# Optimization experiments

Measured on AMD Instinct MI355X. Metric: run time of the kernel, lower is better.

The kernel has to match this reference:

```python
import jax, jax.numpy as jnp
import numpy as np

B, S, D, H, L, K = 16, 512, 256, 8, 4, 16
N, E, NE = B * S, 65536, 32768
DFF = 2 * D
HD = D // H


def _layer_norm(x, g, b):
    mu = jnp.mean(x, axis=-1, keepdims=True)
    var = jnp.mean(jnp.square(x - mu), axis=-1, keepdims=True)
    return (x - mu) / jnp.sqrt(var + 1e-5) * g + b


def setup_inputs() -> dict:
    key = jax.random.key(0)
    ks = iter(jax.random.split(key, 32))
    p = lambda shape: jax.random.normal(next(ks), shape, dtype=jnp.float32) * 0.02
    inp = {
        "node_embedding": jax.random.normal(next(ks), (N, D), dtype=jnp.float32),
        "edge_embedding": jax.random.normal(next(ks), (E, D), dtype=jnp.float32),
        "incidence": jax.random.randint(next(ks), (2, E), 0, N),
        "src_key_padding_mask": jnp.zeros((B, S), dtype=bool),
        "edges_neg": jax.random.randint(next(ks), (NE, 2), 0, N),
        "edges_pos": jax.random.randint(next(ks), (NE, 2), 0, N),
        # ConcatenateLinear(D, D, D): y = x1 @ W1^T + x2 @ W2^T + b
        "msg_w1": p((D, D)), "msg_w2": p((D, D)), "msg_b": p((D,)),
        "pos_table": p((S, D)),
        # per-layer transformer params, stacked on leading L axis
        "in_proj_w": p((L, 3 * D, D)), "in_proj_b": p((L, 3 * D)),
        "out_w": p((L, D, D)), "out_b": p((L, D)),
        "ln1_g": jnp.ones((L, D), jnp.float32), "ln1_b": jnp.zeros((L, D), jnp.float32),
        "ff_w1": p((L, DFF, D)), "ff_b1": p((L, DFF)),
        "ff_w2": p((L, D, DFF)), "ff_b2": p((L, D)),
        "ln2_g": jnp.ones((L, D), jnp.float32), "ln2_b": jnp.zeros((L, D), jnp.float32),
        "pe_w": p((1, D)), "pe_b": p((1,)),
        "pt_w": p((K, D)), "pt_b": p((K,)),
    }
    return inp


def reference(node_embedding, edge_embedding, incidence, src_key_padding_mask,
              edges_neg, edges_pos, msg_w1, msg_w2, msg_b, pos_table,
              in_proj_w, in_proj_b, out_w, out_b, ln1_g, ln1_b,
              ff_w1, ff_b1, ff_w2, ff_b2, ln2_g, ln2_b,
              pe_w, pe_b, pt_w, pt_b):
    # --- aggregate_by_incidence: gather -> ConcatenateLinear -> scatter-add ---
    msgs = (node_embedding[incidence[1]] @ msg_w1.T
            + edge_embedding @ msg_w2.T + msg_b)            # [E, D]
    agreg = jnp.zeros_like(node_embedding).at[incidence[0]].add(msgs)

    # positional encoding tiled over the batch (positions = arange(lMax))
    x = node_embedding + agreg + jnp.tile(pos_table, (B, 1))
    x = x.reshape(B, S, D)

    mask_bias = jnp.where(src_key_padding_mask, -1e9, 0.0)[:, None, None, :]  # [B,1,1,S]
    scale = 1.0 / jnp.sqrt(jnp.float32(HD))

    # post-norm TransformerEncoder (dropout=0 at eval), relu FFN
    for i in range(L):
        wq, wk, wv = jnp.split(in_proj_w[i], 3, axis=0)
        bq, bk, bv = jnp.split(in_proj_b[i], 3, axis=0)
        q = (x @ wq.T + bq).reshape(B, S, H, HD)
        k = (x @ wk.T + bk).reshape(B, S, H, HD)
        v = (x @ wv.T + bv).reshape(B, S, H, HD)
        scores = jnp.einsum('bqhd,bkhd->bhqk', q, k) * scale + mask_bias
        a = jax.nn.softmax(scores, axis=-1)
        o = jnp.einsum('bhqk,bkhd->bqhd', a, v).reshape(B, S, D)
        o = o @ out_w[i].T + out_b[i]
        x = _layer_norm(x + o, ln1_g[i], ln1_b[i])
        h = jax.nn.relu(x @ ff_w1[i].T + ff_b1[i]) @ ff_w2[i].T + ff_b2[i]
        x = _layer_norm(x + h, ln2_g[i], ln2_b[i])

    # --- representation_final_edges: gather pairs, elementwise product ---
    flat = x.reshape(B * S, D)
    rep_pos = flat[edges_pos[:, 0]] * flat[edges_pos[:, 1]]
    rep_neg = flat[edges_neg[:, 0]] * flat[edges_neg[:, 1]]

    pred_pos = rep_pos @ pe_w.T + pe_b      # [NE, 1]
    pred_neg = rep_neg @ pe_w.T + pe_b      # [NE, 1]
    pred_type = rep_pos @ pt_w.T + pt_b     # [NE, K]
    return (pred_pos, pred_neg, pred_type)
```

## Files before the change

kernel.cpp:

```cpp
#include <hip/hip_runtime.h>
#include <hip/hip_bf16.h>

#define B_  16
#define S_  512
#define D_  256
#define H_  8
#define L_  4
#define K_  16
#define N_  (B_ * S_)
#define E_  65536
#define NE_ 32768
#define DFF_ 512
#define HD_ 32

typedef __attribute__((ext_vector_type(8))) __bf16 bf16x8;
typedef __attribute__((ext_vector_type(4))) __bf16 bf16x4;
typedef __attribute__((ext_vector_type(4))) float f32x4;

__device__ __forceinline__ void gl2lds16(const void* g, void* l) {
    __builtin_amdgcn_global_load_lds(
        (const __attribute__((address_space(1))) unsigned int*)g,
        (__attribute__((address_space(3))) unsigned int*)l, 16, 0, 0);
}

#define QSCALE 0.17677669529663688f

__global__ __launch_bounds__(256) void convert_all(
    const float* __restrict__ ipw, __bf16* __restrict__ ipw_bf,
    const float* __restrict__ ow,  __bf16* __restrict__ ow_bf,
    const float* __restrict__ fw1, __bf16* __restrict__ fw1_bf,
    const float* __restrict__ fw2, __bf16* __restrict__ fw2_bf,
    const float* __restrict__ mw1, const float* __restrict__ mw2,
    __bf16* __restrict__ wcat_bf,
    const float* __restrict__ ptw, const float* __restrict__ pew,
    __bf16* __restrict__ wp_bf,
    const float* __restrict__ ipb, float* __restrict__ ipb_s,
    int* __restrict__ cnt)
{
    int blk = blockIdx.x;
    if (blk < 768) {
        size_t i = ((size_t)blk * 256 + threadIdx.x) * 4;
        int row = (int)((i >> 8) % 768);
        float sc = (row < 256) ? QSCALE : 1.0f;
        float4 v = *(const float4*)(ipw + i);
        bf16x4 o = {(__bf16)(v.x * sc), (__bf16)(v.y * sc),
                    (__bf16)(v.z * sc), (__bf16)(v.w * sc)};
        *(bf16x4*)(ipw_bf + i) = o;
    } else if (blk < 2048) {
        const float* src; __bf16* dst; int base;
        if      (blk < 1024)  { src = ow;   dst = ow_bf;   base = blk - 768; }
        else if (blk < 1536)  { src = fw1;  dst = fw1_bf;  base = blk - 1024; }
        else                  { src = fw2;  dst = fw2_bf;  base = blk - 1536; }
        size_t i = ((size_t)base * 256 + threadIdx.x) * 4;
        float4 v = *(const float4*)(src + i);
        bf16x4 o = {(__bf16)v.x, (__bf16)v.y, (__bf16)v.z, (__bf16)v.w};
        *(bf16x4*)(dst + i) = o;
    } else if (blk < 2176) {
        int isw2 = blk >= 2112;
        int base = blk - (isw2 ? 2112 : 2048);
        const float* src = isw2 ? mw2 : mw1;
        size_t i = ((size_t)base * 256 + threadIdx.x) * 4;
        int row = i >> 8, col = i & 255;
        float4 v = *(const float4*)(src + i);
        bf16x4 o = {(__bf16)v.x, (__bf16)v.y, (__bf16)v.z, (__bf16)v.w};
        *(bf16x4*)(wcat_bf + (size_t)row * 512 + (isw2 ? 256 : 0) + col) = o;
    } else if (blk < 2184) {
        int base = blk - 2176;
        size_t i = ((size_t)base * 256 + threadIdx.x) * 4;
        int row = i >> 8, col = i & 255;
        float4 v = make_float4(0.f, 0.f, 0.f, 0.f);
        if (row < 16)       v = *(const float4*)(ptw + row * 256 + col);
        else if (row == 16) v = *(const float4*)(pew + col);
        bf16x4 o = {(__bf16)v.x, (__bf16)v.y, (__bf16)v.z, (__bf16)v.w};
        *(bf16x4*)(wp_bf + i) = o;
    } else if (blk < 2187) {
        int base = blk - 2184;
        size_t i = ((size_t)base * 256 + threadIdx.x) * 4;
        if (i < 3072) {
            float sc = ((i % 768) < 256) ? QSCALE : 1.0f;
            float4 v = *(const float4*)(ipb + i);
            *(float4*)(ipb_s + i) = make_float4(v.x * sc, v.y * sc, v.z * sc, v.w * sc);
        }
    } else {
        int base = blk - 2187;
        int4* p = (int4*)(cnt + ((size_t)base * 256 + threadIdx.x) * 4);
        *p = make_int4(0, 0, 0, 0);
    }
}

__global__ __launch_bounds__(256) void hist_kernel(
    const int* __restrict__ inc, int* __restrict__ cnt)
{
    int e = blockIdx.x * 256 + threadIdx.x;
    atomicAdd(&cnt[inc[e]], 1);
}

__global__ __launch_bounds__(256) void scan_kernel(
    const int* __restrict__ cnt, int* __restrict__ row_ptr, int* __restrict__ ofs)
{
    __shared__ int part[256];
    int t = threadIdx.x;
    int base = t * 32, sum = 0;
    int local[32];
    #pragma unroll
    for (int j = 0; j < 32; ++j) { local[j] = cnt[base + j]; sum += local[j]; }
    part[t] = sum;
    __syncthreads();
    #pragma unroll
    for (int off = 1; off < 256; off <<= 1) {
        int other = (t >= off) ? part[t - off] : 0;
        __syncthreads();
        part[t] += other;
        __syncthreads();
    }
    int run = part[t] - sum;
    for (int j = 0; j < 32; ++j) {
        row_ptr[base + j] = run;
        ofs[base + j] = run;
        run += local[j];
    }
    if (t == 255) row_ptr[8192] = run;
}

__global__ __launch_bounds__(256) void fill_kernel(
    const int* __restrict__ inc, int* __restrict__ ofs, int* __restrict__ elist)
{
    int e = blockIdx.x * 256 + threadIdx.x;
    int pos = atomicAdd(&ofs[inc[e]], 1);
    elist[pos] = e;
}

__global__ __launch_bounds__(256) void csr_gather(
    const float* __restrict__ node, const float* __restrict__ edge,
    const int* __restrict__ inc, const int* __restrict__ row_ptr,
    const int* __restrict__ elist, __bf16* __restrict__ G)
{
    int n = blockIdx.x * 4 + (threadIdx.x >> 6);
    int lane = threadIdx.x & 63;
    int s = row_ptr[n], epos = row_ptr[n + 1];
    float4 an = {0.f, 0.f, 0.f, 0.f}, ae = {0.f, 0.f, 0.f, 0.f};
    int i = s;
    for (; i + 2 <= epos; i += 2) {
        int e0 = elist[i], e1 = elist[i + 1];
        int s0 = inc[E_ + e0], s1 = inc[E_ + e1];
        float4 nv0 = *(const float4*)(node + (size_t)s0 * 256 + lane * 4);
        float4 ev0 = *(const float4*)(edge + (size_t)e0 * 256 + lane * 4);
        float4 nv1 = *(const float4*)(node + (size_t)s1 * 256 + lane * 4);
        float4 ev1 = *(const float4*)(edge + (size_t)e1 * 256 + lane * 4);
        an.x += nv0.x + nv1.x; an.y += nv0.y + nv1.y;
        an.z += nv0.z + nv1.z; an.w += nv0.w + nv1.w;
        ae.x += ev0.x + ev1.x; ae.y += ev0.y + ev1.y;
        ae.z += ev0.z + ev1.z; ae.w += ev0.w + ev1.w;
    }
    if (i < epos) {
        int e0 = elist[i];
        int s0 = inc[E_ + e0];
        float4 nv0 = *(const float4*)(node + (size_t)s0 * 256 + lane * 4);
        float4 ev0 = *(const float4*)(edge + (size_t)e0 * 256 + lane * 4);
        an.x += nv0.x; an.y += nv0.y; an.z += nv0.z; an.w += nv0.w;
        ae.x += ev0.x; ae.y += ev0.y; ae.z += ev0.z; ae.w += ev0.w;
    }
    __bf16* g = G + (size_t)n * 512 + lane * 4;
    bf16x4 bn = {(__bf16)an.x, (__bf16)an.y, (__bf16)an.z, (__bf16)an.w};
    bf16x4 be = {(__bf16)ae.x, (__bf16)ae.y, (__bf16)ae.z, (__bf16)ae.w};
    *(bf16x4*)g = bn;
    *(bf16x4*)(g + 256) = be;
}

template <typename OutT>
__global__ __launch_bounds__(256) void gemm_mfma(
    const __bf16* __restrict__ A, const __bf16* __restrict__ Bw,
    const float* __restrict__ bias, OutT* __restrict__ C,
    int M, int N, int Kd, int relu)
{
    __shared__ __bf16 As0[64 * 32], As1[64 * 32];
    __shared__ __bf16 Bs0[128 * 32], Bs1[128 * 32];
    int tid = threadIdx.x;
    int m0 = blockIdx.y * 64, n0 = blockIdx.x * 128;
    int w = tid >> 6, lane = tid & 63, quad = lane >> 4, r16 = lane & 15;
    int wr = w >> 1, wc = w & 1;

    int lr = tid >> 2, lc = (tid & 3) * 8;
    const __bf16* ag  = A  + (size_t)(m0 + lr) * Kd + lc;
    const __bf16* bg0 = Bw + (size_t)(n0 + lr) * Kd + lc;
    const __bf16* bg1 = bg0 + (size_t)64 * Kd;

    f32x4 acc[2][4] = {};

    for (int k0 = 0; k0 < Kd; k0 += 64) {
        __syncthreads();
        gl2lds16(ag + k0,        As0 + tid * 8);
        gl2lds16(ag + k0 + 32,   As1 + tid * 8);
        gl2lds16(bg0 + k0,       Bs0 + tid * 8);
        gl2lds16(bg1 + k0,       Bs0 + 2048 + tid * 8);
        gl2lds16(bg0 + k0 + 32,  Bs1 + tid * 8);
        gl2lds16(bg1 + k0 + 32,  Bs1 + 2048 + tid * 8);
        __syncthreads();

        #pragma unroll
        for (int kh = 0; kh < 2; ++kh) {
            const __bf16* Asr = kh ? As1 : As0;
            const __bf16* Bsr = kh ? Bs1 : Bs0;
            bf16x8 af[2], bfr[4];
            #pragma unroll
            for (int mt = 0; mt < 2; ++mt)
                af[mt] = *(const bf16x8*)(Asr + (wr * 32 + mt * 16 + r16) * 32 + quad * 8);
            #pragma unroll
            for (int nt = 0; nt < 4; ++nt)
                bfr[nt] = *(const bf16x8*)(Bsr + (wc * 64 + nt * 16 + r16) * 32 + quad * 8);
            #pragma unroll
            for (int mt = 0; mt < 2; ++mt)
                #pragma unroll
                for (int nt = 0; nt < 4; ++nt)
                    acc[mt][nt] = __builtin_amdgcn_mfma_f32_16x16x32_bf16(
                        af[mt], bfr[nt], acc[mt][nt], 0, 0, 0);
        }
    }

    #pragma unroll
    for (int nt = 0; nt < 4; ++nt) {
        int n = n0 + wc * 64 + nt * 16 + r16;
        float bv = bias[n];
        #pragma unroll
        for (int mt = 0; mt < 2; ++mt) {
            #pragma unroll
            for (int reg = 0; reg < 4; ++reg) {
                int m = m0 + wr * 32 + mt * 16 + quad * 4 + reg;
                float v = acc[mt][nt][reg] + bv;
                if (relu) v = fmaxf(v, 0.f);
                C[(size_t)m * N + n] = (OutT)v;
            }
        }
    }
}

__global__ __launch_bounds__(256) void agreg_gemm(
    const __bf16* __restrict__ G, const __bf16* __restrict__ Wc,
    const int* __restrict__ row_ptr, const float* __restrict__ mb,
    const float* __restrict__ node, const float* __restrict__ pos,
    float* __restrict__ xo, __bf16* __restrict__ xo_bf)
{
    __shared__ __bf16 As0[32 * 32], As1[32 * 32];
    __shared__ __bf16 Bs0[128 * 32], Bs1[128 * 32];
    int tid = threadIdx.x;
    int m0 = blockIdx.y * 32, n0 = blockIdx.x * 128;
    int w = tid >> 6, lane = tid & 63, quad = lane >> 4, r16 = lane & 15;
    int wr = w >> 1, wc = w & 1;

    int lr = tid >> 2, lc = (tid & 3) * 8;
    const __bf16* ag  = G  + (size_t)(m0 + (tid >> 2 & 31)) * 512 + lc;
    const __bf16* bg0 = Wc + (size_t)(n0 + lr) * 512 + lc;
    const __bf16* bg1 = bg0 + (size_t)64 * 512;

    f32x4 acc[4] = {};

    for (int k0 = 0; k0 < 512; k0 += 64) {
        __syncthreads();
        if (tid < 128) {
            gl2lds16(ag + k0,      As0 + tid * 8);
            gl2lds16(ag + k0 + 32, As1 + tid * 8);
        }
        gl2lds16(bg0 + k0,       Bs0 + tid * 8);
        gl2lds16(bg1 + k0,       Bs0 + 2048 + tid * 8);
        gl2lds16(bg0 + k0 + 32,  Bs1 + tid * 8);
        gl2lds16(bg1 + k0 + 32,  Bs1 + 2048 + tid * 8);
        __syncthreads();

        #pragma unroll
        for (int kh = 0; kh < 2; ++kh) {
            const __bf16* Asr = kh ? As1 : As0;
            const __bf16* Bsr = kh ? Bs1 : Bs0;
            bf16x8 af = *(const bf16x8*)(Asr + (wr * 16 + r16) * 32 + quad * 8);
            #pragma unroll
            for (int nt = 0; nt < 4; ++nt) {
                bf16x8 bfr = *(const bf16x8*)(Bsr + (wc * 64 + nt * 16 + r16) * 32 + quad * 8);
                acc[nt] = __builtin_amdgcn_mfma_f32_16x16x32_bf16(af, bfr, acc[nt], 0, 0, 0);
            }
        }
    }

    #pragma unroll
    for (int nt = 0; nt < 4; ++nt) {
        int n = n0 + wc * 64 + nt * 16 + r16;
        float mbv = mb[n];
        #pragma unroll
        for (int reg = 0; reg < 4; ++reg) {
            int m = m0 + wr * 16 + quad * 4 + reg;
            float deg = (float)(row_ptr[m + 1] - row_ptr[m]);
            float v = acc[nt][reg] + deg * mbv
                    + node[(size_t)m * 256 + n] + pos[(size_t)(m & 511) * 256 + n];
            xo[(size_t)m * 256 + n] = v;
            xo_bf[(size_t)m * 256 + n] = (__bf16)v;
        }
    }
}

__global__ __launch_bounds__(256) void gemm_ln(
    const __bf16* __restrict__ A, const __bf16* __restrict__ W,
    const float* __restrict__ bias, const float* res,
    const float* __restrict__ g, const float* __restrict__ b,
    float* xo, __bf16* __restrict__ xo_bf, int Kd)
{
    __shared__ __bf16 As0[16 * 32], As1[16 * 32];
    __shared__ __bf16 Bs0[256 * 32], Bs1[256 * 32];
    __shared__ float redS[4][16], redQ[4][16];
    int tid = threadIdx.x;
    int m0 = blockIdx.x * 16;
    int w = tid >> 6, lane = tid & 63, quad = lane >> 4, r16 = lane & 15;

    f32x4 acc[4] = {};

    for (int k0 = 0; k0 < Kd; k0 += 64) {
        __syncthreads();
        if (tid < 64) {
            const __bf16* ap = A + (size_t)(m0 + (tid >> 2)) * Kd + (tid & 3) * 8;
            gl2lds16(ap + k0,      As0 + tid * 8);
            gl2lds16(ap + k0 + 32, As1 + tid * 8);
        }
        #pragma unroll
        for (int c = 0; c < 4; ++c) {
            const __bf16* wp = W + (size_t)(c * 64 + (tid >> 2)) * Kd + (tid & 3) * 8;
            gl2lds16(wp + k0,      Bs0 + c * 2048 + tid * 8);
            gl2lds16(wp + k0 + 32, Bs1 + c * 2048 + tid * 8);
        }
        __syncthreads();

        #pragma unroll
        for (int kh = 0; kh < 2; ++kh) {
            const __bf16* Asr = kh ? As1 : As0;
            const __bf16* Bsr = kh ? Bs1 : Bs0;
            bf16x8 af = *(const bf16x8*)(Asr + r16 * 32 + quad * 8);
            #pragma unroll
            for (int nt = 0; nt < 4; ++nt) {
                bf16x8 bfr = *(const bf16x8*)(Bsr + (w * 64 + nt * 16 + r16) * 32 + quad * 8);
                acc[nt] = __builtin_amdgcn_mfma_f32_16x16x32_bf16(af, bfr, acc[nt], 0, 0, 0);
            }
        }
    }

    float vv[4][4];
    float ls[4], lq[4];
    #pragma unroll
    for (int reg = 0; reg < 4; ++reg) {
        int m = m0 + quad * 4 + reg;
        float s = 0.f, q = 0.f;
        #pragma unroll
        for (int nt = 0; nt < 4; ++nt) {
            int col = w * 64 + nt * 16 + r16;
            float val = acc[nt][reg] + bias[col] + res[(size_t)m * 256 + col];
            vv[reg][nt] = val;
            s += val; q += val * val;
        }
        #pragma unroll
        for (int off = 1; off < 16; off <<= 1) {
            s += __shfl_xor(s, off);
            q += __shfl_xor(q, off);
        }
        ls[reg] = s; lq[reg] = q;
    }
    if (r16 == 0) {
        #pragma unroll
        for (int reg = 0; reg < 4; ++reg) {
            int r = quad * 4 + reg;
            redS[w][r] = ls[reg];
            redQ[w][r] = lq[reg];
        }
    }
    __syncthreads();

    #pragma unroll
    for (int reg = 0; reg < 4; ++reg) {
        int r = quad * 4 + reg;
        int m = m0 + r;
        float s = redS[0][r] + redS[1][r] + redS[2][r] + redS[3][r];
        float q = redQ[0][r] + redQ[1][r] + redQ[2][r] + redQ[3][r];
        float mu = s * (1.f / 256.f);
        float var = q * (1.f / 256.f) - mu * mu;
        float rstd = rsqrtf(var + 1e-5f);
        #pragma unroll
        for (int nt = 0; nt < 4; ++nt) {
            int col = w * 64 + nt * 16 + r16;
            float val = (vv[reg][nt] - mu) * rstd * g[col] + b[col];
            xo[(size_t)m * 256 + col] = val;
            xo_bf[(size_t)m * 256 + col] = (__bf16)val;
        }
    }
}

#define VS 72
#define PS 72

__global__ __launch_bounds__(256) void attn_mfma_kernel(
    const __bf16* __restrict__ qkv, __bf16* __restrict__ o)
{
    __shared__ __bf16 Vt[2][32 * VS];
    __shared__ __bf16 Ps[4][16 * PS];

    int tid  = threadIdx.x;
    int w    = tid >> 6, lane = tid & 63;
    int quad = lane >> 4, r16 = lane & 15;
    int qt = blockIdx.x;
    int bh = blockIdx.y;
    int b = bh >> 3, h = bh & 7;
    int base = b * S_;
    int q0 = qt * 64;

    bf16x8 qa = *(const bf16x8*)(
        qkv + (size_t)(base + q0 + w * 16 + r16) * 768 + h * 32 + quad * 8);

    int kp  = tid & 31;
    int cch = (tid >> 5) & 3;
    int jh  = tid >> 7;
    const __bf16* vbase = qkv + (size_t)base * 768 + 512 + h * 32 + cch * 8;
    const __bf16* kbase = qkv + (size_t)base * 768 + 256 + h * 32 + quad * 8;

    bf16x8 va  = *(const bf16x8*)(vbase + (size_t)(2 * kp) * 768);
    bf16x8 vb2 = *(const bf16x8*)(vbase + (size_t)(2 * kp + 1) * 768);
    bf16x8 kb[4], kbn[4];
    #pragma unroll
    for (int t = 0; t < 4; ++t)
        kbn[t] = *(const bf16x8*)(kbase + (size_t)(t * 16 + r16) * 768);

    f32x4 oacc0 = {0.f, 0.f, 0.f, 0.f};
    f32x4 oacc1 = {0.f, 0.f, 0.f, 0.f};
    float l_i[4] = {0.f, 0.f, 0.f, 0.f};

    for (int kt = 0; kt < 8; ++kt) {
        int buf = kt & 1;
        #pragma unroll
        for (int j = 0; j < 4; ++j) {
            int jj = jh * 4 + j;
            int d = cch * 8 + jj;
            union { __bf16 hh[2]; unsigned int u; } pk;
            pk.hh[0] = va[jj];
            pk.hh[1] = vb2[jj];
            *(unsigned int*)(&Vt[buf][d * VS + 2 * kp]) = pk.u;
        }
        #pragma unroll
        for (int t = 0; t < 4; ++t) kb[t] = kbn[t];
        __syncthreads();

        if (kt < 7) {
            int off = (kt + 1) * 64;
            va  = *(const bf16x8*)(vbase + (size_t)(off + 2 * kp) * 768);
            vb2 = *(const bf16x8*)(vbase + (size_t)(off + 2 * kp + 1) * 768);
            #pragma unroll
            for (int t = 0; t < 4; ++t)
                kbn[t] = *(const bf16x8*)(kbase + (size_t)(off + t * 16 + r16) * 768);
        }

        f32x4 s[4];
        #pragma unroll
        for (int t = 0; t < 4; ++t)
            s[t] = __builtin_amdgcn_mfma_f32_16x16x32_bf16(
                qa, kb[t], (f32x4){0.f, 0.f, 0.f, 0.f}, 0, 0, 0);

        #pragma unroll
        for (int r = 0; r < 4; ++r) {
            float p0 = __expf(s[0][r]), p1 = __expf(s[1][r]);
            float p2 = __expf(s[2][r]), p3 = __expf(s[3][r]);
            l_i[r] += (p0 + p1) + (p2 + p3);
            __bf16* pw = &Ps[w][(quad * 4 + r) * PS + r16];
            pw[0]  = (__bf16)p0;
            pw[16] = (__bf16)p1;
            pw[32] = (__bf16)p2;
            pw[48] = (__bf16)p3;
        }

        #pragma unroll
        for (int c = 0; c < 2; ++c) {
            bf16x8 pa  = *(const bf16x8*)(&Ps[w][r16 * PS + c * 32 + quad * 8]);
            bf16x8 vb0 = *(const bf16x8*)(&Vt[buf][r16 * VS + c * 32 + quad * 8]);
            bf16x8 vb1 = *(const bf16x8*)(&Vt[buf][(16 + r16) * VS + c * 32 + quad * 8]);
            oacc0 = __builtin_amdgcn_mfma_f32_16x16x32_bf16(pa, vb0, oacc0, 0, 0, 0);
            oacc1 = __builtin_amdgcn_mfma_f32_16x16x32_bf16(pa, vb1, oacc1, 0, 0, 0);
        }
    }

    #pragma unroll
    for (int r = 0; r < 4; ++r) {
        float ls = l_i[r];
        #pragma unroll
        for (int off = 1; off < 16; off <<= 1) ls += __shfl_xor(ls, off);
        float inv = 1.0f / ls;
        int q = base + q0 + w * 16 + quad * 4 + r;
        __bf16* op = o + (size_t)q * 256 + h * 32;
        op[r16]      = (__bf16)(oacc0[r] * inv);
        op[16 + r16] = (__bf16)(oacc1[r] * inv);
    }
}

#define PP 264

__global__ __launch_bounds__(256) void pred_mfma(
    const __bf16* __restrict__ xbf, const int* __restrict__ ep,
    const int* __restrict__ en, const __bf16* __restrict__ Wp,
    const float* __restrict__ pe_b, const float* __restrict__ pt_b,
    float* __restrict__ out)
{
    __shared__ __bf16 P[4][16 * PP];
    int tid = threadIdx.x;
    int w = tid >> 6, lane = tid & 63, quad = lane >> 4, r16 = lane & 15;
    int isPos = blockIdx.x < 512;
    int e0 = (blockIdx.x & 511) * 64 + w * 16;
    const int* epair = isPos ? ep : en;

    int half = lane >> 5;
    int col = (lane & 31) * 8;
    #pragma unroll
    for (int j = 0; j < 8; ++j) {
        int je = j * 2 + half;
        int e = e0 + je;
        int a = epair[2 * e], c = epair[2 * e + 1];
        bf16x8 av = *(const bf16x8*)(xbf + (size_t)a * 256 + col);
        bf16x8 cv = *(const bf16x8*)(xbf + (size_t)c * 256 + col);
        bf16x8 pv;
        #pragma unroll
        for (int t = 0; t < 8; ++t)
            pv[t] = (__bf16)((float)av[t] * (float)cv[t]);
        *(bf16x8*)(&P[w][je * PP + col]) = pv;
    }
    __syncthreads();

    f32x4 acc1 = {0.f, 0.f, 0.f, 0.f};
    f32x4 acc2 = {0.f, 0.f, 0.f, 0.f};
    #pragma unroll
    for (int k0 = 0; k0 < 256; k0 += 32) {
        bf16x8 af = *(const bf16x8*)(&P[w][r16 * PP + k0 + quad * 8]);
        bf16x8 b2 = *(const bf16x8*)(Wp + (size_t)(16 + r16) * 256 + k0 + quad * 8);
        acc2 = __builtin_amdgcn_mfma_f32_16x16x32_bf16(af, b2, acc2, 0, 0, 0);
        if (isPos) {
            bf16x8 b1 = *(const bf16x8*)(Wp + (size_t)r16 * 256 + k0 + quad * 8);
            acc1 = __builtin_amdgcn_mfma_f32_16x16x32_bf16(af, b1, acc1, 0, 0, 0);
        }
    }

    float* pred_pos = out;
    float* pred_neg = out + NE_;
    float* pred_type = out + 2 * NE_;
    float peb = pe_b[0];
    if (isPos) {
        float ptbv = pt_b[r16];
        #pragma unroll
        for (int reg = 0; reg < 4; ++reg) {
            int e = e0 + quad * 4 + reg;
            pred_type[(size_t)e * 16 + r16] = acc1[reg] + ptbv;
        }
        if (r16 == 0) {
            #pragma unroll
            for (int reg = 0; reg < 4; ++reg)
                pred_pos[e0 + quad * 4 + reg] = acc2[reg] + peb;
        }
    } else {
        if (r16 == 0) {
            #pragma unroll
            for (int reg = 0; reg < 4; ++reg)
                pred_neg[e0 + quad * 4 + reg] = acc2[reg] + peb;
        }
    }
}

extern "C" void kernel_launch(void* const* d_in, const int* in_sizes, int n_in,
                              void* d_out, int out_size, void* d_ws, size_t ws_size,
                              hipStream_t stream)
{
    const float* node_emb  = (const float*)d_in[0];
    const float* edge_emb  = (const float*)d_in[1];
    const int*   incidence = (const int*)d_in[2];
    const int*   edges_neg = (const int*)d_in[4];
    const int*   edges_pos = (const int*)d_in[5];
    const float* msg_w1    = (const float*)d_in[6];
    const float* msg_w2    = (const float*)d_in[7];
    const float* msg_b     = (const float*)d_in[8];
    const float* pos_table = (const float*)d_in[9];
    const float* in_proj_w = (const float*)d_in[10];
    const float* in_proj_b = (const float*)d_in[11];
    const float* out_w     = (const float*)d_in[12];
    const float* out_b     = (const float*)d_in[13];
    const float* ln1_g     = (const float*)d_in[14];
    const float* ln1_b     = (const float*)d_in[15];
    const float* ff_w1     = (const float*)d_in[16];
    const float* ff_b1     = (const float*)d_in[17];
    const float* ff_w2     = (const float*)d_in[18];
    const float* ff_b2     = (const float*)d_in[19];
    const float* ln2_g     = (const float*)d_in[20];
    const float* ln2_b     = (const float*)d_in[21];
    const float* pe_w      = (const float*)d_in[22];
    const float* pe_b      = (const float*)d_in[23];
    const float* pt_w      = (const float*)d_in[24];
    const float* pt_b      = (const float*)d_in[25];

    float*  x       = (float*)d_ws;
    __bf16* x_bf    = (__bf16*)(x + (size_t)N_ * D_);
    __bf16* ipw_bf  = x_bf + (size_t)N_ * D_;
    __bf16* ow_bf   = ipw_bf + 786432;
    __bf16* fw1_bf  = ow_bf + 262144;
    __bf16* fw2_bf  = fw1_bf + 524288;
    __bf16* wcat_bf = fw2_bf + 524288;
    __bf16* wp_bf   = wcat_bf + 131072;
    float*  ipb_s   = (float*)(wp_bf + 8192);
    float*  scratch = ipb_s + 3072;
    int*    cnt     = (int*)scratch;
    int*    row_ptr = cnt + 8192;
    int*    ofs     = row_ptr + 8200;
    int*    elist   = ofs + 8192;
    __bf16* qkv_bf = (__bf16*)scratch;
    __bf16* o_bf   = qkv_bf + (size_t)N_ * 768;
    __bf16* h_bf   = o_bf + (size_t)N_ * D_;
    __bf16* G_bf   = (__bf16*)(scratch + 6291456);

    convert_all<<<2195, 256, 0, stream>>>(
        in_proj_w, ipw_bf, out_w, ow_bf, ff_w1, fw1_bf, ff_w2, fw2_bf,
        msg_w1, msg_w2, wcat_bf, pt_w, pe_w, wp_bf, in_proj_b, ipb_s, cnt);

    hist_kernel<<<E_ / 256, 256, 0, stream>>>(incidence, cnt);
    scan_kernel<<<1, 256, 0, stream>>>(cnt, row_ptr, ofs);
    fill_kernel<<<E_ / 256, 256, 0, stream>>>(incidence, ofs, elist);

    csr_gather<<<N_ / 4, 256, 0, stream>>>(
        node_emb, edge_emb, incidence, row_ptr, elist, G_bf);
    agreg_gemm<<<dim3(2, N_ / 32), 256, 0, stream>>>(
        G_bf, wcat_bf, row_ptr, msg_b, node_emb, pos_table, x, x_bf);

    for (int li = 0; li < L_; ++li) {
        gemm_mfma<__bf16><<<dim3(768 / 128, N_ / 64), 256, 0, stream>>>(
            x_bf, ipw_bf + (size_t)li * 768 * 256, ipb_s + li * 768,
            qkv_bf, N_, 768, 256, 0);
        attn_mfma_kernel<<<dim3(S_ / 64, B_ * H_), 256, 0, stream>>>(qkv_bf, o_bf);
        gemm_ln<<<N_ / 16, 256, 0, stream>>>(
            o_bf, ow_bf + (size_t)li * 256 * 256, out_b + li * 256,
            x, ln1_g + li * 256, ln1_b + li * 256, x, x_bf, 256);
        gemm_mfma<__bf16><<<dim3(512 / 128, N_ / 64), 256, 0, stream>>>(
            x_bf, fw1_bf + (size_t)li * 512 * 256, ff_b1 + li * 512,
            h_bf, N_, 512, 256, 1);
        gemm_ln<<<N_ / 16, 256, 0, stream>>>(
            h_bf, fw2_bf + (size_t)li * 256 * 512, ff_b2 + li * 256,
            x, ln2_g + li * 256, ln2_b + li * 256, x, x_bf, 512);
    }

    pred_mfma<<<1024, 256, 0, stream>>>(
        x_bf, edges_pos, edges_neg, wp_bf, pe_b, pt_b, (float*)d_out);
}
```

Before: 465.7 us.

## Fuse out-proj+LN1, FFN up/relu, FFN down+LN2 into one per-row-tile kernel

Replaces the out-projection+LN kernel, the FFN1 GEMM and the FFN2+LN kernel with a single kernel. Each block processes 16 rows and keeps the LN1 output and the ReLU hidden activations in LDS, so the hidden tensor no longer round-trips through global memory and two launches per layer disappear. It also skips the fp32 x write on the last layer, where only the bf16 copy is read afterwards. In exchange, each 16-row block reloads all of W1 and W2 from global/L2 with no reuse across rows, and the larger LDS footprint may lower occupancy.

```diff
diff --git a/kernel.cpp b/kernel.cpp
--- a/kernel.cpp
+++ b/kernel.cpp
@@ -295,40 +295,49 @@
     }
 }
 
-__global__ __launch_bounds__(256) void gemm_ln(
-    const __bf16* __restrict__ A, const __bf16* __restrict__ W,
-    const float* __restrict__ bias, const float* res,
-    const float* __restrict__ g, const float* __restrict__ b,
-    float* xo, __bf16* __restrict__ xo_bf, int Kd)
-{
+__global__ __launch_bounds__(256) void tail_fused(
+    const __bf16* __restrict__ A,
+    const __bf16* __restrict__ Wo,
+    const float* __restrict__ ob,
+    const float* __restrict__ res,
+    const float* __restrict__ g1, const float* __restrict__ b1,
+    const __bf16* __restrict__ W1,
+    const float* __restrict__ fb1,
+    const __bf16* __restrict__ W2,
+    const float* __restrict__ fb2,
+    const float* __restrict__ g2, const float* __restrict__ b2,
+    float* __restrict__ xo, __bf16* __restrict__ xo_bf, int wx32)
+{
+    __shared__ __bf16 Bs[512 * 32];
     __shared__ __bf16 As0[16 * 32], As1[16 * 32];
-    __shared__ __bf16 Bs0[256 * 32], Bs1[256 * 32];
+    __shared__ __bf16 x1s[16 * 264];
+    __shared__ __bf16 hs[16 * 520];
     __shared__ float redS[4][16], redQ[4][16];
+
     int tid = threadIdx.x;
     int m0 = blockIdx.x * 16;
     int w = tid >> 6, lane = tid & 63, quad = lane >> 4, r16 = lane & 15;
 
     f32x4 acc[4] = {};
-
-    for (int k0 = 0; k0 < Kd; k0 += 64) {
+    for (int k0 = 0; k0 < 256; k0 += 64) {
         __syncthreads();
         if (tid < 64) {
-            const __bf16* ap = A + (size_t)(m0 + (tid >> 2)) * Kd + (tid & 3) * 8;
+            const __bf16* ap = A + (size_t)(m0 + (tid >> 2)) * 256 + (tid & 3) * 8;
             gl2lds16(ap + k0,      As0 + tid * 8);
             gl2lds16(ap + k0 + 32, As1 + tid * 8);
         }
         #pragma unroll
         for (int c = 0; c < 4; ++c) {
-            const __bf16* wp = W + (size_t)(c * 64 + (tid >> 2)) * Kd + (tid & 3) * 8;
-            gl2lds16(wp + k0,      Bs0 + c * 2048 + tid * 8);
-            gl2lds16(wp + k0 + 32, Bs1 + c * 2048 + tid * 8);
+            const __bf16* wp = Wo + (size_t)(c * 64 + (tid >> 2)) * 256 + (tid & 3) * 8;
+            gl2lds16(wp + k0,      Bs + c * 2048 + tid * 8);
+            gl2lds16(wp + k0 + 32, Bs + 8192 + c * 2048 + tid * 8);
         }
         __syncthreads();
 
         #pragma unroll
         for (int kh = 0; kh < 2; ++kh) {
             const __bf16* Asr = kh ? As1 : As0;
-            const __bf16* Bsr = kh ? Bs1 : Bs0;
+            const __bf16* Bsr = Bs + kh * 8192;
             bf16x8 af = *(const bf16x8*)(Asr + r16 * 32 + quad * 8);
             #pragma unroll
             for (int nt = 0; nt < 4; ++nt) {
@@ -338,51 +347,150 @@
         }
     }
 
-    float vv[4][4];
-    float ls[4], lq[4];
-    #pragma unroll
-    for (int reg = 0; reg < 4; ++reg) {
-        int m = m0 + quad * 4 + reg;
-        float s = 0.f, q = 0.f;
-        #pragma unroll
-        for (int nt = 0; nt < 4; ++nt) {
-            int col = w * 64 + nt * 16 + r16;
-            float val = acc[nt][reg] + bias[col] + res[(size_t)m * 256 + col];
-            vv[reg][nt] = val;
-            s += val; q += val * val;
-        }
-        #pragma unroll
-        for (int off = 1; off < 16; off <<= 1) {
-            s += __shfl_xor(s, off);
-            q += __shfl_xor(q, off);
-        }
-        ls[reg] = s; lq[reg] = q;
-    }
-    if (r16 == 0) {
+    float vv1[4][4];
+    {
+        float ls[4], lq[4];
+        #pragma unroll
+        for (int reg = 0; reg < 4; ++reg) {
+            int m = m0 + quad * 4 + reg;
+            float s = 0.f, q = 0.f;
+            #pragma unroll
+            for (int nt = 0; nt < 4; ++nt) {
+                int col = w * 64 + nt * 16 + r16;
+                float val = acc[nt][reg] + ob[col] + res[(size_t)m * 256 + col];
+                vv1[reg][nt] = val;
+                s += val; q += val * val;
+            }
+            #pragma unroll
+            for (int off = 1; off < 16; off <<= 1) {
+                s += __shfl_xor(s, off);
+                q += __shfl_xor(q, off);
+            }
+            ls[reg] = s; lq[reg] = q;
+        }
+        if (r16 == 0) {
+            #pragma unroll
+            for (int reg = 0; reg < 4; ++reg) {
+                int r = quad * 4 + reg;
+                redS[w][r] = ls[reg];
+                redQ[w][r] = lq[reg];
+            }
+        }
+        __syncthreads();
         #pragma unroll
         for (int reg = 0; reg < 4; ++reg) {
             int r = quad * 4 + reg;
-            redS[w][r] = ls[reg];
-            redQ[w][r] = lq[reg];
-        }
-    }
-    __syncthreads();
-
-    #pragma unroll
-    for (int reg = 0; reg < 4; ++reg) {
-        int r = quad * 4 + reg;
-        int m = m0 + r;
-        float s = redS[0][r] + redS[1][r] + redS[2][r] + redS[3][r];
-        float q = redQ[0][r] + redQ[1][r] + redQ[2][r] + redQ[3][r];
-        float mu = s * (1.f / 256.f);
-        float var = q * (1.f / 256.f) - mu * mu;
-        float rstd = rsqrtf(var + 1e-5f);
-        #pragma unroll
-        for (int nt = 0; nt < 4; ++nt) {
-            int col = w * 64 + nt * 16 + r16;
-            float val = (vv[reg][nt] - mu) * rstd * g[col] + b[col];
-            xo[(size_t)m * 256 + col] = val;
-            xo_bf[(size_t)m * 256 + col] = (__bf16)val;
+            float s = redS[0][r] + redS[1][r] + redS[2][r] + redS[3][r];
+            float q = redQ[0][r] + redQ[1][r] + redQ[2][r] + redQ[3][r];
+            float mu = s * (1.f / 256.f);
+            float var = q * (1.f / 256.f) - mu * mu;
+            float rstd = rsqrtf(var + 1e-5f);
+            #pragma unroll
+            for (int nt = 0; nt < 4; ++nt) {
+                int col = w * 64 + nt * 16 + r16;
+                float val = (vv1[reg][nt] - mu) * rstd * g1[col] + b1[col];
+                vv1[reg][nt] = val;
+                x1s[r * 264 + col] = (__bf16)val;
+            }
+        }
+    }
+
+    f32x4 hacc[8] = {};
+    for (int k0 = 0; k0 < 256; k0 += 32) {
+        __syncthreads();
+        {
+            const __bf16* wp = W1 + (size_t)(tid >> 2) * 256 + (tid & 3) * 8 + k0;
+            #pragma unroll
+            for (int j = 0; j < 8; ++j)
+                gl2lds16(wp + (size_t)j * 64 * 256, Bs + j * 2048 + tid * 8);
+        }
+        __syncthreads();
+        bf16x8 af = *(const bf16x8*)(x1s + r16 * 264 + k0 + quad * 8);
+        #pragma unroll
+        for (int nt = 0; nt < 8; ++nt) {
+            bf16x8 bfr = *(const bf16x8*)(Bs + (w * 128 + nt * 16 + r16) * 32 + quad * 8);
+            hacc[nt] = __builtin_amdgcn_mfma_f32_16x16x32_bf16(af, bfr, hacc[nt], 0, 0, 0);
+        }
+    }
+    #pragma unroll
+    for (int nt = 0; nt < 8; ++nt) {
+        int col = w * 128 + nt * 16 + r16;
+        float bb = fb1[col];
+        #pragma unroll
+        for (int reg = 0; reg < 4; ++reg) {
+            float v = fmaxf(hacc[nt][reg] + bb, 0.f);
+            hs[(quad * 4 + reg) * 520 + col] = (__bf16)v;
+        }
+    }
+
+    f32x4 cacc[4] = {};
+    for (int k0 = 0; k0 < 512; k0 += 64) {
+        __syncthreads();
+        #pragma unroll
+        for (int c = 0; c < 4; ++c) {
+            const __bf16* wp = W2 + (size_t)(c * 64 + (tid >> 2)) * 512 + (tid & 3) * 8;
+            gl2lds16(wp + k0,      Bs + c * 2048 + tid * 8);
+            gl2lds16(wp + k0 + 32, Bs + 8192 + c * 2048 + tid * 8);
+        }
+        __syncthreads();
+        #pragma unroll
+        for (int kh = 0; kh < 2; ++kh) {
+            const __bf16* Bsr = Bs + kh * 8192;
+            bf16x8 af = *(const bf16x8*)(hs + r16 * 520 + k0 + kh * 32 + quad * 8);
+            #pragma unroll
+            for (int nt = 0; nt < 4; ++nt) {
+                bf16x8 bfr = *(const bf16x8*)(Bsr + (w * 64 + nt * 16 + r16) * 32 + quad * 8);
+                cacc[nt] = __builtin_amdgcn_mfma_f32_16x16x32_bf16(af, bfr, cacc[nt], 0, 0, 0);
+            }
+        }
+    }
+
+    {
+        float vvc[4][4];
+        float ls[4], lq[4];
+        #pragma unroll
+        for (int reg = 0; reg < 4; ++reg) {
+            float s = 0.f, q = 0.f;
+            #pragma unroll
+            for (int nt = 0; nt < 4; ++nt) {
+                int col = w * 64 + nt * 16 + r16;
+                float val = cacc[nt][reg] + fb2[col] + vv1[reg][nt];
+                vvc[reg][nt] = val;
+                s += val; q += val * val;
+            }
+            #pragma unroll
+            for (int off = 1; off < 16; off <<= 1) {
+                s += __shfl_xor(s, off);
+                q += __shfl_xor(q, off);
+            }
+            ls[reg] = s; lq[reg] = q;
+        }
+        __syncthreads();
+        if (r16 == 0) {
+            #pragma unroll
+            for (int reg = 0; reg < 4; ++reg) {
+                int r = quad * 4 + reg;
+                redS[w][r] = ls[reg];
+                redQ[w][r] = lq[reg];
+            }
+        }
+        __syncthreads();
+        #pragma unroll
+        for (int reg = 0; reg < 4; ++reg) {
+            int r = quad * 4 + reg;
+            int m = m0 + r;
+            float s = redS[0][r] + redS[1][r] + redS[2][r] + redS[3][r];
+            float q = redQ[0][r] + redQ[1][r] + redQ[2][r] + redQ[3][r];
+            float mu = s * (1.f / 256.f);
+            float var = q * (1.f / 256.f) - mu * mu;
+            float rstd = rsqrtf(var + 1e-5f);
+            #pragma unroll
+            for (int nt = 0; nt < 4; ++nt) {
+                int col = w * 64 + nt * 16 + r16;
+                float val = (vvc[reg][nt] - mu) * rstd * g2[col] + b2[col];
+                if (wx32) xo[(size_t)m * 256 + col] = val;
+                xo_bf[(size_t)m * 256 + col] = (__bf16)val;
+            }
         }
     }
 }
@@ -606,7 +714,6 @@
     int*    elist   = ofs + 8192;
     __bf16* qkv_bf = (__bf16*)scratch;
     __bf16* o_bf   = qkv_bf + (size_t)N_ * 768;
-    __bf16* h_bf   = o_bf + (size_t)N_ * D_;
     __bf16* G_bf   = (__bf16*)(scratch + 6291456);
 
     convert_all<<<2195, 256, 0, stream>>>(
@@ -627,15 +734,13 @@
             x_bf, ipw_bf + (size_t)li * 768 * 256, ipb_s + li * 768,
             qkv_bf, N_, 768, 256, 0);
         attn_mfma_kernel<<<dim3(S_ / 64, B_ * H_), 256, 0, stream>>>(qkv_bf, o_bf);
-        gemm_ln<<<N_ / 16, 256, 0, stream>>>(
+        tail_fused<<<N_ / 16, 256, 0, stream>>>(
             o_bf, ow_bf + (size_t)li * 256 * 256, out_b + li * 256,
-            x, ln1_g + li * 256, ln1_b + li * 256, x, x_bf, 256);
-        gemm_mfma<__bf16><<<dim3(512 / 128, N_ / 64), 256, 0, stream>>>(
-            x_bf, fw1_bf + (size_t)li * 512 * 256, ff_b1 + li * 512,
-            h_bf, N_, 512, 256, 1);
-        gemm_ln<<<N_ / 16, 256, 0, stream>>>(
-            h_bf, fw2_bf + (size_t)li * 256 * 512, ff_b2 + li * 256,
-            x, ln2_g + li * 256, ln2_b + li * 256, x, x_bf, 512);
+            x, ln1_g + li * 256, ln1_b + li * 256,
+            fw1_bf + (size_t)li * 512 * 256, ff_b1 + li * 512,
+            fw2_bf + (size_t)li * 256 * 512, ff_b2 + li * 256,
+            ln2_g + li * 256, ln2_b + li * 256,
+            x, x_bf, li == L_ - 1 ? 0 : 1);
     }
 
     pred_mfma<<<1024, 256, 0, stream>>>(
```

Result: faster. 442.2 us (-5.0%).
